# Performance work log

Hardware: AMD Instinct MI355X
Metric: run time of the kernel (lower is better)

## Reference

```python
import jax, jax.numpy as jnp
import numpy as np

NUM_HEAD = 8
HIDDEN = 1024


def setup_inputs() -> dict:
    key = jax.random.key(0)
    ks = jax.random.split(key, 7)
    B, Q, K = 2, 256, 256
    return {
        "query": jax.random.normal(ks[0], (B, Q, HIDDEN), jnp.float32),
        "keys": jax.random.normal(ks[1], (B, K, HIDDEN), jnp.float32),
        "values": jax.random.normal(ks[2], (B, K, HIDDEN), jnp.float32),
        "mask": jax.random.randint(ks[3], (B, K), 0, 2, jnp.int32),
        "W_q": jax.random.normal(ks[4], (HIDDEN, HIDDEN), jnp.float32),
        "W_k": jax.random.normal(ks[5], (HIDDEN, HIDDEN), jnp.float32),
        "V_a": jax.random.normal(ks[6], (HIDDEN,), jnp.float32),
    }


def reference(query, keys, values, mask, W_q, W_k, V_a):
    B, Q, H = query.shape
    K = keys.shape[1]
    h_q = query @ W_q                                   # [B,Q,H]
    h_k = keys @ W_k                                    # [B,K,H]
    # additive (Bahdanau) scores, split hidden into heads and sum per head
    h = jnp.tanh(h_q[:, :, None, :] + h_k[:, None, :, :]) * V_a   # [B,Q,K,H]
    logits = h.reshape(B, Q, K, NUM_HEAD, H // NUM_HEAD).sum(-1)  # [B,Q,K,h]
    logits = jnp.transpose(logits, (0, 3, 1, 2))        # [B,h,Q,K]
    penalty = (1.0 - mask.astype(jnp.float32)) * 99.0   # [B,K]
    logits = logits - penalty[:, None, None, :]
    weights = jax.nn.softmax(logits, axis=-1)           # [B,h,Q,K]
    v = values.reshape(B, K, NUM_HEAD, H // NUM_HEAD)   # [B,K,h,d]
    ctx = jnp.einsum('bhqk,bkhd->bqhd', weights, v).reshape(B, Q, H)
    return ctx, weights
```

## Files before the change

### kernel.cpp

```cpp
#include <hip/hip_runtime.h>
#include <hip/hip_bf16.h>


#define TANH_SCALE 2.88539008177792681472f
#define LOG2E      1.44269504088896340736f

typedef __attribute__((ext_vector_type(8))) short bf16x8_t;
typedef __attribute__((ext_vector_type(4))) float f32x4_t;

__device__ inline ushort bf16_rne(float f) {
  unsigned u = __float_as_uint(f);
  u += 0x7FFFu + ((u >> 16) & 1u);
  return (ushort)(u >> 16);
}
__device__ inline float bf16_to_f(ushort h) { return __uint_as_float((unsigned)h << 16); }
__device__ inline void split1(float v, ushort& hi, ushort& lo) {
  hi = bf16_rne(v);
  lo = bf16_rne(v - bf16_to_f(hi));
}

__global__ __launch_bounds__(256) void prep(
    const float* __restrict__ query, const float* __restrict__ keys,
    const float* __restrict__ Wq, const float* __restrict__ Wk,
    ushort* __restrict__ qhi, ushort* __restrict__ qlo,
    ushort* __restrict__ khi, ushort* __restrict__ klo,
    ushort* __restrict__ wqthi, ushort* __restrict__ wqtlo,
    ushort* __restrict__ wkthi, ushort* __restrict__ wktlo)
{
  __shared__ float t[64][65];
  const int bid = blockIdx.x, tid = threadIdx.x;
  if (bid < 1024) {
    const int z = bid >> 9;
    const float* in = z ? keys : query;
    ushort* hi = z ? khi : qhi;
    ushort* lo = z ? klo : qlo;
    const size_t i = ((size_t)(bid & 511) * 256 + tid) * 4;
    float4 v = *(const float4*)(in + i);
    ushort h0, h1, h2, h3, l0, l1, l2, l3;
    split1(v.x, h0, l0); split1(v.y, h1, l1);
    split1(v.z, h2, l2); split1(v.w, h3, l3);
    *(ushort4*)(hi + i) = make_ushort4(h0, h1, h2, h3);
    *(ushort4*)(lo + i) = make_ushort4(l0, l1, l2, l3);
  } else {
    const int idx = bid - 1024;
    const int z = idx >> 8;
    const float* W = z ? Wk : Wq;
    ushort* thi = z ? wkthi : wqthi;
    ushort* tlo = z ? wktlo : wqtlo;
    const int n0 = (idx & 15) * 64, h0 = ((idx >> 4) & 15) * 64;
    const int r = tid >> 4, c = (tid & 15) * 4;
#pragma unroll
    for (int i = 0; i < 4; ++i) {
      const int rr = r + i * 16;
      float4 wv = *(const float4*)(W + (size_t)(h0 + rr) * 1024 + n0 + c);
      t[rr][c + 0] = wv.x; t[rr][c + 1] = wv.y;
      t[rr][c + 2] = wv.z; t[rr][c + 3] = wv.w;
    }
    __syncthreads();
#pragma unroll
    for (int i = 0; i < 4; ++i) {
      const int rr = r + i * 16;
      ushort h0v, h1v, h2v, h3v, l0v, l1v, l2v, l3v;
      split1(t[c + 0][rr] * TANH_SCALE, h0v, l0v);
      split1(t[c + 1][rr] * TANH_SCALE, h1v, l1v);
      split1(t[c + 2][rr] * TANH_SCALE, h2v, l2v);
      split1(t[c + 3][rr] * TANH_SCALE, h3v, l3v);
      *(ushort4*)(thi + (size_t)(n0 + rr) * 1024 + h0 + c) = make_ushort4(h0v, h1v, h2v, h3v);
      *(ushort4*)(tlo + (size_t)(n0 + rr) * 1024 + h0 + c) = make_ushort4(l0v, l1v, l2v, l3v);
    }
  }
}

__global__ __launch_bounds__(256) void gemm_mfma(
    const ushort* __restrict__ qhi, const ushort* __restrict__ qlo,
    const ushort* __restrict__ khi, const ushort* __restrict__ klo,
    const ushort* __restrict__ wqthi, const ushort* __restrict__ wqtlo,
    const ushort* __restrict__ wkthi, const ushort* __restrict__ wktlo,
    float* __restrict__ hq_f, float* __restrict__ hkT)
{
  const int z = blockIdx.y;
  const int bid = blockIdx.x;
  int m0, n0, ldc;
  const ushort *Ah_g, *Al_g, *Bh_g, *Bl_g;
  float* C;
  if (z == 0) {
    m0 = (bid >> 4) * 64; n0 = (bid & 15) * 64; ldc = 1024;
    Ah_g = qhi; Al_g = qlo; Bh_g = wqthi; Bl_g = wqtlo; C = hq_f;
  } else {
    m0 = (bid >> 3) * 64; n0 = (bid & 7) * 64; ldc = 512;
    Ah_g = wkthi; Al_g = wktlo; Bh_g = khi; Bl_g = klo; C = hkT;
  }

  __shared__ __align__(16) ushort Ah[64 * 40];
  __shared__ __align__(16) ushort Al[64 * 40];
  __shared__ __align__(16) ushort Bh[64 * 40];
  __shared__ __align__(16) ushort Bl[64 * 40];

  const int tid = threadIdx.x;
  const int srow = tid >> 2, skc = (tid & 3) * 8;
  const size_t gA = (size_t)(m0 + srow) * 1024 + skc;
  const size_t gB = (size_t)(n0 + srow) * 1024 + skc;
  const int soff = srow * 40 + skc;

  uint4 rah = *(const uint4*)(Ah_g + gA);
  uint4 ral = *(const uint4*)(Al_g + gA);
  uint4 rbh = *(const uint4*)(Bh_g + gB);
  uint4 rbl = *(const uint4*)(Bl_g + gB);

  const int w = __builtin_amdgcn_readfirstlane(tid >> 6);
  const int lane = tid & 63;
  const int wm = (w >> 1) * 32, wn = (w & 1) * 32;
  const int fr = lane & 15, kg = lane >> 4;
  const int aoff = (wm + fr) * 40 + kg * 8;
  const int boff = (wn + fr) * 40 + kg * 8;

  f32x4_t acc[2][2] = {};

  for (int kk = 0; kk < 1024; kk += 32) {
    __syncthreads();
    *(uint4*)(Ah + soff) = rah;
    *(uint4*)(Al + soff) = ral;
    *(uint4*)(Bh + soff) = rbh;
    *(uint4*)(Bl + soff) = rbl;
    __syncthreads();

    if (kk + 32 < 1024) {
      rah = *(const uint4*)(Ah_g + gA + kk + 32);
      ral = *(const uint4*)(Al_g + gA + kk + 32);
      rbh = *(const uint4*)(Bh_g + gB + kk + 32);
      rbl = *(const uint4*)(Bl_g + gB + kk + 32);
    }

    bf16x8_t ah0 = *(const bf16x8_t*)(Ah + aoff);
    bf16x8_t ah1 = *(const bf16x8_t*)(Ah + aoff + 16 * 40);
    bf16x8_t al0 = *(const bf16x8_t*)(Al + aoff);
    bf16x8_t al1 = *(const bf16x8_t*)(Al + aoff + 16 * 40);
    bf16x8_t bh0 = *(const bf16x8_t*)(Bh + boff);
    bf16x8_t bh1 = *(const bf16x8_t*)(Bh + boff + 16 * 40);
    bf16x8_t bl0 = *(const bf16x8_t*)(Bl + boff);
    bf16x8_t bl1 = *(const bf16x8_t*)(Bl + boff + 16 * 40);

    acc[0][0] = __builtin_amdgcn_mfma_f32_16x16x32_bf16(ah0, bh0, acc[0][0], 0, 0, 0);
    acc[0][1] = __builtin_amdgcn_mfma_f32_16x16x32_bf16(ah0, bh1, acc[0][1], 0, 0, 0);
    acc[1][0] = __builtin_amdgcn_mfma_f32_16x16x32_bf16(ah1, bh0, acc[1][0], 0, 0, 0);
    acc[1][1] = __builtin_amdgcn_mfma_f32_16x16x32_bf16(ah1, bh1, acc[1][1], 0, 0, 0);
    acc[0][0] = __builtin_amdgcn_mfma_f32_16x16x32_bf16(ah0, bl0, acc[0][0], 0, 0, 0);
    acc[0][1] = __builtin_amdgcn_mfma_f32_16x16x32_bf16(ah0, bl1, acc[0][1], 0, 0, 0);
    acc[1][0] = __builtin_amdgcn_mfma_f32_16x16x32_bf16(ah1, bl0, acc[1][0], 0, 0, 0);
    acc[1][1] = __builtin_amdgcn_mfma_f32_16x16x32_bf16(ah1, bl1, acc[1][1], 0, 0, 0);
    acc[0][0] = __builtin_amdgcn_mfma_f32_16x16x32_bf16(al0, bh0, acc[0][0], 0, 0, 0);
    acc[0][1] = __builtin_amdgcn_mfma_f32_16x16x32_bf16(al0, bh1, acc[0][1], 0, 0, 0);
    acc[1][0] = __builtin_amdgcn_mfma_f32_16x16x32_bf16(al1, bh0, acc[1][0], 0, 0, 0);
    acc[1][1] = __builtin_amdgcn_mfma_f32_16x16x32_bf16(al1, bh1, acc[1][1], 0, 0, 0);
  }

#pragma unroll
  for (int fm = 0; fm < 2; ++fm)
#pragma unroll
    for (int fn = 0; fn < 2; ++fn) {
      const int col = n0 + wn + fn * 16 + fr;
#pragma unroll
      for (int j = 0; j < 4; ++j) {
        const int row = m0 + wm + fm * 16 + kg * 4 + j;
        C[(size_t)row * ldc + col] = acc[fm][fn][j];
      }
    }
}

#define TT(hqv, hkv, vav, accq)                                     \
  {                                                                 \
    float a_ = (hqv) + (hkv);                                       \
    float e_ = __builtin_amdgcn_exp2f(a_);                          \
    accq += (vav) * __builtin_amdgcn_rcpf(e_ + 1.0f);               \
  }

__global__ __launch_bounds__(256) void attn_fused(
    const float* __restrict__ hq_f, const float* __restrict__ hkT,
    const float* __restrict__ Va, const int* __restrict__ mask,
    const float* __restrict__ values,
    float* __restrict__ weights, float* __restrict__ ctx)
{
  __shared__ float red_m[4][8];
  __shared__ float red_s[4][8];
  __shared__ __align__(16) float P_lds[8][256];

  const int tid = threadIdx.x;
  const int lane = tid & 63;
  const int w = __builtin_amdgcn_readfirstlane(tid >> 6);
  const int bid = blockIdx.x;
  const int bh = bid >> 5;
  const int b = bh & 1, h = bh >> 1;
  const int qt = (bid & 31) * 8;
  const int k = w * 64 + lane;

  const float pen = 99.0f * (1.0f - (float)mask[b * 256 + k]);

  float ssum = Va[h * 128 + lane] + Va[h * 128 + 64 + lane];
#pragma unroll
  for (int off = 32; off; off >>= 1) ssum += __shfl_xor(ssum, off, 64);

  const float* hkp = hkT + (size_t)(h * 128) * 512 + b * 256 + k;
  const float* hqb = hq_f + (size_t)(b * 256 + qt) * 1024 + h * 128;
  const float* vap = Va + h * 128;

  float acc[8] = {0.f, 0.f, 0.f, 0.f, 0.f, 0.f, 0.f, 0.f};

  float hkc[16], vac[16];
#pragma unroll
  for (int j = 0; j < 16; ++j) hkc[j] = hkp[(size_t)j * 512];
#pragma unroll
  for (int j = 0; j < 16; ++j) vac[j] = vap[j];

  for (int ch = 0; ch < 8; ++ch) {
    const int d0 = ch * 16;
    float hkn[16], van[16];
    if (ch < 7) {
#pragma unroll
      for (int j = 0; j < 16; ++j) hkn[j] = hkp[(size_t)(d0 + 16 + j) * 512];
#pragma unroll
      for (int j = 0; j < 16; ++j) van[j] = vap[d0 + 16 + j];
    }
#pragma unroll
    for (int q = 0; q < 8; ++q) {
      const float* hqq = hqb + (size_t)q * 1024 + d0;
      float4 a0 = *(const float4*)(hqq + 0);
      float4 a1 = *(const float4*)(hqq + 4);
      float4 a2 = *(const float4*)(hqq + 8);
      float4 a3 = *(const float4*)(hqq + 12);
      TT(a0.x, hkc[0],  vac[0],  acc[q]);
      TT(a0.y, hkc[1],  vac[1],  acc[q]);
      TT(a0.z, hkc[2],  vac[2],  acc[q]);
      TT(a0.w, hkc[3],  vac[3],  acc[q]);
      TT(a1.x, hkc[4],  vac[4],  acc[q]);
      TT(a1.y, hkc[5],  vac[5],  acc[q]);
      TT(a1.z, hkc[6],  vac[6],  acc[q]);
      TT(a1.w, hkc[7],  vac[7],  acc[q]);
      TT(a2.x, hkc[8],  vac[8],  acc[q]);
      TT(a2.y, hkc[9],  vac[9],  acc[q]);
      TT(a2.z, hkc[10], vac[10], acc[q]);
      TT(a2.w, hkc[11], vac[11], acc[q]);
      TT(a3.x, hkc[12], vac[12], acc[q]);
      TT(a3.y, hkc[13], vac[13], acc[q]);
      TT(a3.z, hkc[14], vac[14], acc[q]);
      TT(a3.w, hkc[15], vac[15], acc[q]);
    }
    if (ch < 7) {
#pragma unroll
      for (int j = 0; j < 16; ++j) { hkc[j] = hkn[j]; vac[j] = van[j]; }
    }
  }

  float l[8], p[8];
#pragma unroll
  for (int q = 0; q < 8; ++q) l[q] = ssum - 2.0f * acc[q] - pen;

#pragma unroll
  for (int q = 0; q < 8; ++q) {
    float m = l[q];
#pragma unroll
    for (int off = 32; off; off >>= 1) m = fmaxf(m, __shfl_xor(m, off, 64));
    if (lane == 0) red_m[w][q] = m;
  }
  __syncthreads();
#pragma unroll
  for (int q = 0; q < 8; ++q) {
    float m = fmaxf(fmaxf(red_m[0][q], red_m[1][q]), fmaxf(red_m[2][q], red_m[3][q]));
    p[q] = __builtin_amdgcn_exp2f((l[q] - m) * LOG2E);
  }
#pragma unroll
  for (int q = 0; q < 8; ++q) {
    float s = p[q];
#pragma unroll
    for (int off = 32; off; off >>= 1) s += __shfl_xor(s, off, 64);
    if (lane == 0) red_s[w][q] = s;
  }
  __syncthreads();
#pragma unroll
  for (int q = 0; q < 8; ++q) {
    const float s = (red_s[0][q] + red_s[1][q]) + (red_s[2][q] + red_s[3][q]);
    const float pq = p[q] / s;
    weights[((size_t)((b * 8 + h) * 256) + qt + q) * 256 + k] = pq;
    P_lds[q][k] = pq;
  }
  __syncthreads();

  const int d4 = lane & 31, ks = lane >> 5;
  const int q0 = w * 2, q1 = q0 + 1;
  const float* vb = values + (size_t)(b * 256 + ks * 128) * 1024 + h * 128 + d4 * 4;
  float4 A0 = make_float4(0, 0, 0, 0), A1 = make_float4(0, 0, 0, 0);
#pragma unroll 2
  for (int k4 = 0; k4 < 32; ++k4) {
    float4 p0v = *(const float4*)&P_lds[q0][ks * 128 + k4 * 4];
    float4 p1v = *(const float4*)&P_lds[q1][ks * 128 + k4 * 4];
#pragma unroll
    for (int j = 0; j < 4; ++j) {
      float4 v = *(const float4*)(vb + (size_t)(k4 * 4 + j) * 1024);
      const float pj0 = (j == 0) ? p0v.x : (j == 1) ? p0v.y : (j == 2) ? p0v.z : p0v.w;
      const float pj1 = (j == 0) ? p1v.x : (j == 1) ? p1v.y : (j == 2) ? p1v.z : p1v.w;
      A0.x += pj0 * v.x; A0.y += pj0 * v.y; A0.z += pj0 * v.z; A0.w += pj0 * v.w;
      A1.x += pj1 * v.x; A1.y += pj1 * v.y; A1.z += pj1 * v.z; A1.w += pj1 * v.w;
    }
  }
  A0.x += __shfl_xor(A0.x, 32, 64); A0.y += __shfl_xor(A0.y, 32, 64);
  A0.z += __shfl_xor(A0.z, 32, 64); A0.w += __shfl_xor(A0.w, 32, 64);
  A1.x += __shfl_xor(A1.x, 32, 64); A1.y += __shfl_xor(A1.y, 32, 64);
  A1.z += __shfl_xor(A1.z, 32, 64); A1.w += __shfl_xor(A1.w, 32, 64);
  if (lane < 32) {
    *(float4*)&ctx[(size_t)(b * 256 + qt + q0) * 1024 + h * 128 + d4 * 4] = A0;
    *(float4*)&ctx[(size_t)(b * 256 + qt + q1) * 1024 + h * 128 + d4 * 4] = A1;
  }
}

extern "C" void kernel_launch(void* const* d_in, const int* in_sizes, int n_in,
                              void* d_out, int out_size, void* d_ws, size_t ws_size,
                              hipStream_t stream) {
  const float* query  = (const float*)d_in[0];
  const float* keys   = (const float*)d_in[1];
  const float* values = (const float*)d_in[2];
  const int*   mask   = (const int*)d_in[3];
  const float* Wq     = (const float*)d_in[4];
  const float* Wk     = (const float*)d_in[5];
  const float* Va     = (const float*)d_in[6];

  float* ctx     = (float*)d_out;
  float* weights = ctx + 524288;

  ushort* qhi   = (ushort*)d_ws;
  ushort* qlo   = qhi + 524288;
  ushort* khi   = qlo + 524288;
  ushort* klo   = khi + 524288;
  ushort* wqthi = klo + 524288;
  ushort* wqtlo = wqthi + 1048576;
  ushort* wkthi = wqtlo + 1048576;
  ushort* wktlo = wkthi + 1048576;
  float*  hq_f  = (float*)(wktlo + 1048576);
  float*  hkT   = hq_f + 524288;

  prep<<<dim3(1536), 256, 0, stream>>>(query, keys, Wq, Wk,
                                       qhi, qlo, khi, klo,
                                       wqthi, wqtlo, wkthi, wktlo);
  gemm_mfma<<<dim3(128, 2), 256, 0, stream>>>(qhi, qlo, khi, klo,
                                              wqthi, wqtlo, wkthi, wktlo, hq_f, hkT);
  attn_fused<<<dim3(512), 256, 0, stream>>>(hq_f, hkT, Va, mask, values, weights, ctx);
}
```

Before: 75.49 us.

## Precompute exp2 of projections as packed mantissa/exponent to avoid per-element exp

The GEMM epilogue now stores exp2 of each projected value, packed as a 16-bit mantissa and a biased 16-bit exponent. The attention kernel rebuilds exp2(hq+hk) as a product of two mantissas followed by v_ldexp, so the transcendental exp2 in the Q*K*H inner loop becomes a multiply, a few integer ops and an ldexp. This lowers pressure on the transcendental unit, but adds bit-manipulation ALU work. The 16-bit mantissa also loses precision, and the mantissa clamp near 2.0 can introduce error.

```diff
diff --git a/kernel.cpp b/kernel.cpp
--- a/kernel.cpp
+++ b/kernel.cpp
@@ -17,6 +17,20 @@
 __device__ inline void split1(float v, ushort& hi, ushort& lo) {
   hi = bf16_rne(v);
   lo = bf16_rne(v - bf16_to_f(hi));
+}
+
+__device__ inline unsigned pack_exp(float a) {
+  float fa = floorf(a);
+  float m = __builtin_amdgcn_exp2f(a - fa);
+  unsigned mb = __float_as_uint(m);
+  unsigned mant = (mb >= 0x40000000u) ? 0xFFFFu : ((mb >> 7) & 0xFFFFu);
+  return (mant << 16) | (((unsigned)((int)fa + 32768)) & 0xFFFFu);
+}
+
+__device__ inline float ldexp_f(float x, int e) {
+  float r;
+  asm("v_ldexp_f32 %0, %1, %2" : "=v"(r) : "v"(x), "v"(e));
+  return r;
 }
 
 __global__ __launch_bounds__(256) void prep(
@@ -76,19 +90,19 @@
     const ushort* __restrict__ khi, const ushort* __restrict__ klo,
     const ushort* __restrict__ wqthi, const ushort* __restrict__ wqtlo,
     const ushort* __restrict__ wkthi, const ushort* __restrict__ wktlo,
-    float* __restrict__ hq_f, float* __restrict__ hkT)
+    unsigned* __restrict__ PQ, unsigned* __restrict__ PKT)
 {
   const int z = blockIdx.y;
   const int bid = blockIdx.x;
   int m0, n0, ldc;
   const ushort *Ah_g, *Al_g, *Bh_g, *Bl_g;
-  float* C;
+  unsigned* C;
   if (z == 0) {
     m0 = (bid >> 4) * 64; n0 = (bid & 15) * 64; ldc = 1024;
-    Ah_g = qhi; Al_g = qlo; Bh_g = wqthi; Bl_g = wqtlo; C = hq_f;
+    Ah_g = qhi; Al_g = qlo; Bh_g = wqthi; Bl_g = wqtlo; C = PQ;
   } else {
     m0 = (bid >> 3) * 64; n0 = (bid & 7) * 64; ldc = 512;
-    Ah_g = wkthi; Al_g = wktlo; Bh_g = khi; Bl_g = klo; C = hkT;
+    Ah_g = wkthi; Al_g = wktlo; Bh_g = khi; Bl_g = klo; C = PKT;
   }
 
   __shared__ __align__(16) ushort Ah[64 * 40];
@@ -162,20 +176,13 @@
 #pragma unroll
       for (int j = 0; j < 4; ++j) {
         const int row = m0 + wm + fm * 16 + kg * 4 + j;
-        C[(size_t)row * ldc + col] = acc[fm][fn][j];
+        C[(size_t)row * ldc + col] = pack_exp(acc[fm][fn][j]);
       }
     }
 }
 
-#define TT(hqv, hkv, vav, accq)                                     \
-  {                                                                 \
-    float a_ = (hqv) + (hkv);                                       \
-    float e_ = __builtin_amdgcn_exp2f(a_);                          \
-    accq += (vav) * __builtin_amdgcn_rcpf(e_ + 1.0f);               \
-  }
-
 __global__ __launch_bounds__(256) void attn_fused(
-    const float* __restrict__ hq_f, const float* __restrict__ hkT,
+    const unsigned* __restrict__ PQ, const unsigned* __restrict__ PKT,
     const float* __restrict__ Va, const int* __restrict__ mask,
     const float* __restrict__ values,
     float* __restrict__ weights, float* __restrict__ ctx)
@@ -199,54 +206,53 @@
 #pragma unroll
   for (int off = 32; off; off >>= 1) ssum += __shfl_xor(ssum, off, 64);
 
-  const float* hkp = hkT + (size_t)(h * 128) * 512 + b * 256 + k;
-  const float* hqb = hq_f + (size_t)(b * 256 + qt) * 1024 + h * 128;
+  const unsigned* pkp = PKT + (size_t)(h * 128) * 512 + b * 256 + k;
+  const unsigned* pqb = PQ + (size_t)(b * 256 + qt) * 1024 + h * 128;
   const float* vap = Va + h * 128;
 
   float acc[8] = {0.f, 0.f, 0.f, 0.f, 0.f, 0.f, 0.f, 0.f};
 
-  float hkc[16], vac[16];
-#pragma unroll
-  for (int j = 0; j < 16; ++j) hkc[j] = hkp[(size_t)j * 512];
-#pragma unroll
-  for (int j = 0; j < 16; ++j) vac[j] = vap[j];
+  float mkc[16]; int ikc[16]; unsigned pkn[16];
+#pragma unroll
+  for (int j = 0; j < 16; ++j) pkn[j] = pkp[(size_t)j * 512];
+#pragma unroll
+  for (int j = 0; j < 16; ++j) {
+    mkc[j] = __uint_as_float(0x3F800000u | ((pkn[j] >> 16) << 7));
+    ikc[j] = (int)(pkn[j] & 0xFFFFu) - 32768;
+  }
 
   for (int ch = 0; ch < 8; ++ch) {
     const int d0 = ch * 16;
-    float hkn[16], van[16];
     if (ch < 7) {
 #pragma unroll
-      for (int j = 0; j < 16; ++j) hkn[j] = hkp[(size_t)(d0 + 16 + j) * 512];
-#pragma unroll
-      for (int j = 0; j < 16; ++j) van[j] = vap[d0 + 16 + j];
+      for (int j = 0; j < 16; ++j) pkn[j] = pkp[(size_t)(d0 + 16 + j) * 512];
     }
 #pragma unroll
     for (int q = 0; q < 8; ++q) {
-      const float* hqq = hqb + (size_t)q * 1024 + d0;
-      float4 a0 = *(const float4*)(hqq + 0);
-      float4 a1 = *(const float4*)(hqq + 4);
-      float4 a2 = *(const float4*)(hqq + 8);
-      float4 a3 = *(const float4*)(hqq + 12);
-      TT(a0.x, hkc[0],  vac[0],  acc[q]);
-      TT(a0.y, hkc[1],  vac[1],  acc[q]);
-      TT(a0.z, hkc[2],  vac[2],  acc[q]);
-      TT(a0.w, hkc[3],  vac[3],  acc[q]);
-      TT(a1.x, hkc[4],  vac[4],  acc[q]);
-      TT(a1.y, hkc[5],  vac[5],  acc[q]);
-      TT(a1.z, hkc[6],  vac[6],  acc[q]);
-      TT(a1.w, hkc[7],  vac[7],  acc[q]);
-      TT(a2.x, hkc[8],  vac[8],  acc[q]);
-      TT(a2.y, hkc[9],  vac[9],  acc[q]);
-      TT(a2.z, hkc[10], vac[10], acc[q]);
-      TT(a2.w, hkc[11], vac[11], acc[q]);
-      TT(a3.x, hkc[12], vac[12], acc[q]);
-      TT(a3.y, hkc[13], vac[13], acc[q]);
-      TT(a3.z, hkc[14], vac[14], acc[q]);
-      TT(a3.w, hkc[15], vac[15], acc[q]);
+      const unsigned* pqq = pqb + (size_t)q * 1024 + d0;
+#pragma unroll
+      for (int dd = 0; dd < 16; dd += 4) {
+        uint4 pq4 = *(const uint4*)(pqq + dd);
+        float4 va4 = *(const float4*)(vap + d0 + dd);
+#pragma unroll
+        for (int e = 0; e < 4; ++e) {
+          const unsigned pqv = (e == 0) ? pq4.x : (e == 1) ? pq4.y : (e == 2) ? pq4.z : pq4.w;
+          const float vav = (e == 0) ? va4.x : (e == 1) ? va4.y : (e == 2) ? va4.z : va4.w;
+          const float mq = __uint_as_float(0x3F800000u | ((pqv >> 16) << 7));
+          const int iq = (int)(pqv & 0xFFFFu) - 32768;
+          float u_ = mq * mkc[dd + e];
+          int n_ = iq + ikc[dd + e];
+          float t_ = ldexp_f(u_, n_);
+          acc[q] += vav * __builtin_amdgcn_rcpf(t_ + 1.0f);
+        }
+      }
     }
     if (ch < 7) {
 #pragma unroll
-      for (int j = 0; j < 16; ++j) { hkc[j] = hkn[j]; vac[j] = van[j]; }
+      for (int j = 0; j < 16; ++j) {
+        mkc[j] = __uint_as_float(0x3F800000u | ((pkn[j] >> 16) << 7));
+        ikc[j] = (int)(pkn[j] & 0xFFFFu) - 32768;
+      }
     }
   }
 
@@ -333,13 +339,13 @@
   ushort* wqtlo = wqthi + 1048576;
   ushort* wkthi = wqtlo + 1048576;
   ushort* wktlo = wkthi + 1048576;
-  float*  hq_f  = (float*)(wktlo + 1048576);
-  float*  hkT   = hq_f + 524288;
+  unsigned* PQ  = (unsigned*)(wktlo + 1048576);
+  unsigned* PKT = PQ + 524288;
 
   prep<<<dim3(1536), 256, 0, stream>>>(query, keys, Wq, Wk,
                                        qhi, qlo, khi, klo,
                                        wqthi, wqtlo, wkthi, wktlo);
   gemm_mfma<<<dim3(128, 2), 256, 0, stream>>>(qhi, qlo, khi, klo,
-                                              wqthi, wqtlo, wkthi, wktlo, hq_f, hkT);
-  attn_fused<<<dim3(512), 256, 0, stream>>>(hq_f, hkT, Va, mask, values, weights, ctx);
-}
+                                              wqthi, wqtlo, wkthi, wktlo, PQ, PKT);
+  attn_fused<<<dim3(512), 256, 0, stream>>>(PQ, PKT, Va, mask, values, weights, ctx);
+}
```

Result: slower. 86.24 us (+14.2%).

## Factor exp2 of sum into mantissa-exponent products to drop per-element exp

Applied to the files above, without the earlier changes.

The GEMM epilogue now stores each projected value as a mantissa 2^frac and an integer exponent floor(a), so exp2(hq+hk) becomes a multiply plus an integer add and ldexp in the inner attention loop, replacing the transcendental exp2 with cheaper ALU ops. This doubles the intermediate memory traffic, since there are separate float and int arrays for Q and K. It also adds more per-element loads (Va is reloaded per q) and ldexp overflow handling. Accuracy may shift slightly because the mantissa product is rounded differently.

```diff
diff --git a/kernel.cpp b/kernel.cpp
--- a/kernel.cpp
+++ b/kernel.cpp
@@ -76,19 +76,20 @@
     const ushort* __restrict__ khi, const ushort* __restrict__ klo,
     const ushort* __restrict__ wqthi, const ushort* __restrict__ wqtlo,
     const ushort* __restrict__ wkthi, const ushort* __restrict__ wktlo,
-    float* __restrict__ hq_f, float* __restrict__ hkT)
+    float* __restrict__ MQ, int* __restrict__ IQ,
+    float* __restrict__ MKT, int* __restrict__ IKT)
 {
   const int z = blockIdx.y;
   const int bid = blockIdx.x;
   int m0, n0, ldc;
   const ushort *Ah_g, *Al_g, *Bh_g, *Bl_g;
-  float* C;
+  float* Mp; int* Ip;
   if (z == 0) {
     m0 = (bid >> 4) * 64; n0 = (bid & 15) * 64; ldc = 1024;
-    Ah_g = qhi; Al_g = qlo; Bh_g = wqthi; Bl_g = wqtlo; C = hq_f;
+    Ah_g = qhi; Al_g = qlo; Bh_g = wqthi; Bl_g = wqtlo; Mp = MQ; Ip = IQ;
   } else {
     m0 = (bid >> 3) * 64; n0 = (bid & 7) * 64; ldc = 512;
-    Ah_g = wkthi; Al_g = wktlo; Bh_g = khi; Bl_g = klo; C = hkT;
+    Ah_g = wkthi; Al_g = wktlo; Bh_g = khi; Bl_g = klo; Mp = MKT; Ip = IKT;
   }
 
   __shared__ __align__(16) ushort Ah[64 * 40];
@@ -162,20 +163,17 @@
 #pragma unroll
       for (int j = 0; j < 4; ++j) {
         const int row = m0 + wm + fm * 16 + kg * 4 + j;
-        C[(size_t)row * ldc + col] = acc[fm][fn][j];
+        const float a = acc[fm][fn][j];
+        const float fa = floorf(a);
+        Mp[(size_t)row * ldc + col] = __builtin_amdgcn_exp2f(a - fa);
+        Ip[(size_t)row * ldc + col] = (int)fa;
       }
     }
 }
 
-#define TT(hqv, hkv, vav, accq)                                     \
-  {                                                                 \
-    float a_ = (hqv) + (hkv);                                       \
-    float e_ = __builtin_amdgcn_exp2f(a_);                          \
-    accq += (vav) * __builtin_amdgcn_rcpf(e_ + 1.0f);               \
-  }
-
 __global__ __launch_bounds__(256) void attn_fused(
-    const float* __restrict__ hq_f, const float* __restrict__ hkT,
+    const float* __restrict__ MQ, const int* __restrict__ IQ,
+    const float* __restrict__ MKT, const int* __restrict__ IKT,
     const float* __restrict__ Va, const int* __restrict__ mask,
     const float* __restrict__ values,
     float* __restrict__ weights, float* __restrict__ ctx)
@@ -199,54 +197,59 @@
 #pragma unroll
   for (int off = 32; off; off >>= 1) ssum += __shfl_xor(ssum, off, 64);
 
-  const float* hkp = hkT + (size_t)(h * 128) * 512 + b * 256 + k;
-  const float* hqb = hq_f + (size_t)(b * 256 + qt) * 1024 + h * 128;
+  const float* mkp = MKT + (size_t)(h * 128) * 512 + b * 256 + k;
+  const int*   ikp = IKT + (size_t)(h * 128) * 512 + b * 256 + k;
+  const float* mqb = MQ + (size_t)(b * 256 + qt) * 1024 + h * 128;
+  const int*   iqb = IQ + (size_t)(b * 256 + qt) * 1024 + h * 128;
   const float* vap = Va + h * 128;
 
   float acc[8] = {0.f, 0.f, 0.f, 0.f, 0.f, 0.f, 0.f, 0.f};
 
-  float hkc[16], vac[16];
-#pragma unroll
-  for (int j = 0; j < 16; ++j) hkc[j] = hkp[(size_t)j * 512];
-#pragma unroll
-  for (int j = 0; j < 16; ++j) vac[j] = vap[j];
-
-  for (int ch = 0; ch < 8; ++ch) {
-    const int d0 = ch * 16;
-    float hkn[16], van[16];
-    if (ch < 7) {
-#pragma unroll
-      for (int j = 0; j < 16; ++j) hkn[j] = hkp[(size_t)(d0 + 16 + j) * 512];
-#pragma unroll
-      for (int j = 0; j < 16; ++j) van[j] = vap[d0 + 16 + j];
+  float mkc[8]; int ikc[8];
+#pragma unroll
+  for (int j = 0; j < 8; ++j) mkc[j] = mkp[(size_t)j * 512];
+#pragma unroll
+  for (int j = 0; j < 8; ++j) ikc[j] = ikp[(size_t)j * 512];
+
+  for (int ch = 0; ch < 16; ++ch) {
+    const int d0 = ch * 8;
+    float mkn[8]; int ikn[8];
+    if (ch < 15) {
+#pragma unroll
+      for (int j = 0; j < 8; ++j) mkn[j] = mkp[(size_t)(d0 + 8 + j) * 512];
+#pragma unroll
+      for (int j = 0; j < 8; ++j) ikn[j] = ikp[(size_t)(d0 + 8 + j) * 512];
     }
 #pragma unroll
     for (int q = 0; q < 8; ++q) {
-      const float* hqq = hqb + (size_t)q * 1024 + d0;
-      float4 a0 = *(const float4*)(hqq + 0);
-      float4 a1 = *(const float4*)(hqq + 4);
-      float4 a2 = *(const float4*)(hqq + 8);
-      float4 a3 = *(const float4*)(hqq + 12);
-      TT(a0.x, hkc[0],  vac[0],  acc[q]);
-      TT(a0.y, hkc[1],  vac[1],  acc[q]);
-      TT(a0.z, hkc[2],  vac[2],  acc[q]);
-      TT(a0.w, hkc[3],  vac[3],  acc[q]);
-      TT(a1.x, hkc[4],  vac[4],  acc[q]);
-      TT(a1.y, hkc[5],  vac[5],  acc[q]);
-      TT(a1.z, hkc[6],  vac[6],  acc[q]);
-      TT(a1.w, hkc[7],  vac[7],  acc[q]);
-      TT(a2.x, hkc[8],  vac[8],  acc[q]);
-      TT(a2.y, hkc[9],  vac[9],  acc[q]);
-      TT(a2.z, hkc[10], vac[10], acc[q]);
-      TT(a2.w, hkc[11], vac[11], acc[q]);
-      TT(a3.x, hkc[12], vac[12], acc[q]);
-      TT(a3.y, hkc[13], vac[13], acc[q]);
-      TT(a3.z, hkc[14], vac[14], acc[q]);
-      TT(a3.w, hkc[15], vac[15], acc[q]);
-    }
-    if (ch < 7) {
-#pragma unroll
-      for (int j = 0; j < 16; ++j) { hkc[j] = hkn[j]; vac[j] = van[j]; }
+      const float* mqq = mqb + (size_t)q * 1024 + d0;
+      const int*   iqq = iqb + (size_t)q * 1024 + d0;
+      float4 mqa = *(const float4*)(mqq + 0);
+      float4 mqbv = *(const float4*)(mqq + 4);
+      int4 iqa = *(const int4*)(iqq + 0);
+      int4 iqbv = *(const int4*)(iqq + 4);
+      float4 vaa = *(const float4*)(vap + d0 + 0);
+      float4 vab = *(const float4*)(vap + d0 + 4);
+#pragma unroll
+      for (int e = 0; e < 8; ++e) {
+        const float mq = (e == 0) ? mqa.x : (e == 1) ? mqa.y : (e == 2) ? mqa.z :
+                         (e == 3) ? mqa.w : (e == 4) ? mqbv.x : (e == 5) ? mqbv.y :
+                         (e == 6) ? mqbv.z : mqbv.w;
+        const int iq = (e == 0) ? iqa.x : (e == 1) ? iqa.y : (e == 2) ? iqa.z :
+                       (e == 3) ? iqa.w : (e == 4) ? iqbv.x : (e == 5) ? iqbv.y :
+                       (e == 6) ? iqbv.z : iqbv.w;
+        const float va = (e == 0) ? vaa.x : (e == 1) ? vaa.y : (e == 2) ? vaa.z :
+                         (e == 3) ? vaa.w : (e == 4) ? vab.x : (e == 5) ? vab.y :
+                         (e == 6) ? vab.z : vab.w;
+        const float u = mq * mkc[e];
+        const int   n = iq + ikc[e];
+        const float t = ldexpf(u, n);
+        acc[q] += va * __builtin_amdgcn_rcpf(t + 1.0f);
+      }
+    }
+    if (ch < 15) {
+#pragma unroll
+      for (int j = 0; j < 8; ++j) { mkc[j] = mkn[j]; ikc[j] = ikn[j]; }
     }
   }
 
@@ -333,13 +336,17 @@
   ushort* wqtlo = wqthi + 1048576;
   ushort* wkthi = wqtlo + 1048576;
   ushort* wktlo = wkthi + 1048576;
-  float*  hq_f  = (float*)(wktlo + 1048576);
-  float*  hkT   = hq_f + 524288;
+  float*  MQ    = (float*)(wktlo + 1048576);
+  int*    IQ    = (int*)(MQ + 524288);
+  float*  MKT   = (float*)(IQ + 524288);
+  int*    IKT   = (int*)(MKT + 524288);
 
   prep<<<dim3(1536), 256, 0, stream>>>(query, keys, Wq, Wk,
                                        qhi, qlo, khi, klo,
                                        wqthi, wqtlo, wkthi, wktlo);
   gemm_mfma<<<dim3(128, 2), 256, 0, stream>>>(qhi, qlo, khi, klo,
-                                              wqthi, wqtlo, wkthi, wktlo, hq_f, hkT);
-  attn_fused<<<dim3(512), 256, 0, stream>>>(hq_f, hkT, Va, mask, values, weights, ctx);
-}
+                                              wqthi, wqtlo, wkthi, wktlo,
+                                              MQ, IQ, MKT, IKT);
+  attn_fused<<<dim3(512), 256, 0, stream>>>(MQ, IQ, MKT, IKT,
+                                            Va, mask, values, weights, ctx);
+}
```

Result: slower. 83.11 us (+10.1%).
